# Optimization experiments

Hardware: AMD Instinct MI355X
Metric: run time of the kernel (lower is better)

The kernel has to match this reference:

```python
import jax, jax.numpy as jnp
import numpy as np


def _rope_tables(T, half):
    # theta_i = 10000^(-i/half), standard RoPE frequencies for head_size=2*half
    thetas = 10000.0 ** (-jnp.arange(half, dtype=jnp.float32) / half)  # (half,)
    ang = jnp.arange(T, dtype=jnp.float32)[:, None] * thetas[None, :]  # (T, half)
    return jnp.sin(ang), jnp.cos(ang)


def _apply_rope(x, sin, cos):
    # x: (B, H, T, hs); sin/cos: (T, hs//2). Interleaved pair rotation.
    xe = x[..., 0::2]
    xo = x[..., 1::2]
    s = sin[None, None, :, :]
    c = cos[None, None, :, :]
    re = xe * c - xo * s
    ro = xe * s + xo * c
    return jnp.stack([re, ro], axis=-1).reshape(x.shape)


def setup_inputs() -> dict:
    key = jax.random.key(0)
    ks = jax.random.split(key, 5)
    B, T, C, H = 4, 2048, 1024, 16
    scale = 1.0 / np.sqrt(C)
    x = jax.random.normal(ks[0], (B, T, C), dtype=jnp.float32)
    Wqkv = jax.random.normal(ks[1], (C, 3 * C), dtype=jnp.float32) * scale
    bqkv = jax.random.normal(ks[2], (3 * C,), dtype=jnp.float32) * 0.01
    Wout = jax.random.normal(ks[3], (C, C), dtype=jnp.float32) * scale
    bout = jax.random.normal(ks[4], (C,), dtype=jnp.float32) * 0.01
    return {"x": x, "Wqkv": Wqkv, "bqkv": bqkv, "Wout": Wout, "bout": bout,
            "num_heads": H}


def reference(x, Wqkv, bqkv, Wout, bout, num_heads) -> jnp.ndarray:
    B, T, C = x.shape
    H = num_heads
    hs = C // H
    norm = 1.0 / np.sqrt(hs)

    qkv = x @ Wqkv + bqkv                       # (B, T, 3C)
    qkv = qkv.reshape(B, T, 3, H, hs)
    qkv = jnp.transpose(qkv, (0, 3, 2, 1, 4))   # (B, H, 3, T, hs) = transpose(1,3)
    q, k, v = qkv[:, :, 0], qkv[:, :, 1], qkv[:, :, 2]  # each (B, H, T, hs)

    sin, cos = _rope_tables(T, hs // 2)
    q = _apply_rope(q, sin, cos)
    k = _apply_rope(k, sin, cos)

    att = jnp.einsum('bhqd,bhkd->bhqk', q, k) * norm  # (B, H, T, T)
    causal = jnp.triu(jnp.ones((T, T), dtype=bool), k=1)
    att = jnp.where(causal[None, None], -jnp.inf, att)
    att_prob = jax.nn.softmax(att, axis=-1)

    out = jnp.einsum('bhqk,bhkd->bhqd', att_prob, v)  # (B, H, T, hs)
    out = jnp.transpose(out, (0, 2, 1, 3)).reshape(B, T, C)
    return out @ Wout + bout
```

## Files before the change

kernel.cpp:

```cpp
#include <hip/hip_runtime.h>
#include <math.h>

#define B_   4
#define T_   2048
#define C_   1024
#define H_   16
#define HS   64
#define HALF 32
#define QKV_N (3 * C_)
#define M_    (B_ * T_)

using bf16x8 = __attribute__((ext_vector_type(8))) short;
using f32x4  = __attribute__((ext_vector_type(4))) float;
using f32x16 = __attribute__((ext_vector_type(16))) float;
using u16x4  = __attribute__((ext_vector_type(4))) unsigned short;
using u32x2  = __attribute__((ext_vector_type(2))) unsigned int;

__device__ __forceinline__ unsigned short f2bf(float f) {
    unsigned u = __builtin_bit_cast(unsigned, f);
    u = (u + 0x7FFFu + ((u >> 16) & 1u)) >> 16;
    return (unsigned short)u;
}
__device__ __forceinline__ float bf2f(unsigned short b) {
    return __builtin_bit_cast(float, (unsigned)b << 16);
}
__device__ __forceinline__ unsigned cvtpk_bf16(float lo, float hi_) {
    unsigned r;
    asm("v_cvt_pk_bf16_f32 %0, %1, %2" : "=v"(r) : "v"(lo), "v"(hi_));
    return r;
}
__device__ __forceinline__ void gload16(const void* g, void* l) {
    __builtin_amdgcn_global_load_lds(
        (const __attribute__((address_space(1))) unsigned int*)g,
        (__attribute__((address_space(3))) unsigned int*)l, 16, 0, 0);
}
#define WAIT_VMCNT_8() asm volatile("s_waitcnt vmcnt(8)" ::: "memory")
#define WAIT_VMCNT_0() asm volatile("s_waitcnt vmcnt(0)" ::: "memory")

#if __has_builtin(__builtin_amdgcn_exp2f)
#define EXP2(x) __builtin_amdgcn_exp2f(x)
#else
#define EXP2(x) exp2f(x)
#endif
#define FMAX3(a, b, c) fmaxf(fmaxf((a), (b)), (c))

#define QSCALE 0.18033688011112042f

__global__ __launch_bounds__(256) void prep_kernel(
    const float* __restrict__ in, unsigned short* __restrict__ out,
    float2* __restrict__ tab)
{
    const int bid = blockIdx.x;
    if (bid < 4096) {
        const size_t i = ((size_t)bid * 256 + threadIdx.x) * 8;
        const float4 a = *reinterpret_cast<const float4*>(&in[i]);
        const float4 b = *reinterpret_cast<const float4*>(&in[i + 4]);
        bf16x8 v;
        v[0] = f2bf(a.x); v[1] = f2bf(a.y); v[2] = f2bf(a.z); v[3] = f2bf(a.w);
        v[4] = f2bf(b.x); v[5] = f2bf(b.y); v[6] = f2bf(b.z); v[7] = f2bf(b.w);
        *reinterpret_cast<bf16x8*>(&out[i]) = v;
    } else {
        const int idx = (bid - 4096) * 256 + threadIdx.x;
        const int t = idx / HALF;
        const int i = idx % HALF;
        const float theta = powf(10000.0f, -(float)i / (float)HALF);
        const float ang = (float)t * theta;
        float sn, cs;
        sincosf(ang, &sn, &cs);
        tab[idx] = make_float2(sn, cs);
    }
}

__global__ __launch_bounds__(256) void wtrans_kernel(
    const float* __restrict__ Wqkv, const float* __restrict__ Wout,
    unsigned short* __restrict__ Wqkvt, unsigned short* __restrict__ Woutt)
{
    __shared__ float tile[32][33];
    const int bid = blockIdx.x;
    const float* W;
    unsigned short* Wt;
    int N, k0, n0;
    if (bid < 3072) {
        W = Wqkv; Wt = Wqkvt; N = QKV_N;
        n0 = (bid % 96) * 32; k0 = (bid / 96) * 32;
    } else {
        const int r2 = bid - 3072;
        W = Wout; Wt = Woutt; N = C_;
        n0 = (r2 % 32) * 32; k0 = (r2 / 32) * 32;
    }
    const int K = C_;
    const int r = threadIdx.x / 32;
    const int c = threadIdx.x % 32;
    #pragma unroll
    for (int it = 0; it < 4; ++it)
        tile[r + it * 8][c] = W[(size_t)(k0 + r + it * 8) * N + n0 + c];
    __syncthreads();
    #pragma unroll
    for (int it = 0; it < 4; ++it)
        Wt[(size_t)(n0 + r + it * 8) * K + k0 + c] = f2bf(tile[c][r + it * 8]);
}

template <int N, int K, bool BF16OUT, bool ROPE, bool VSPLIT>
__global__ __launch_bounds__(256, 4) void gemm_mfma_kernel(
    const unsigned short* __restrict__ A, const unsigned short* __restrict__ Bt,
    const float* __restrict__ bias, const float2* __restrict__ tab,
    void* __restrict__ Cout, unsigned short* __restrict__ vt, int nbx, int nby)
{
    __shared__ unsigned short As[128 * 32];
    __shared__ unsigned short Bs[128 * 32];

    const int tid  = threadIdx.x;
    const int lane = tid & 63;
    const int wave = tid >> 6;
    const int wr   = wave >> 1;
    const int wc   = wave & 1;
    const int l15  = lane & 15;
    const int l4   = lane >> 4;

    const int bid  = blockIdx.x;
    const int xcd  = bid & 7;
    const int w    = bid >> 3;
    const int cpr  = nbx >> 1;
    const int rpr  = nby >> 2;
    const int by   = ((xcd >> 1) * rpr) + (w / cpr);
    const int bx   = ((xcd & 1) * cpr) + (w % cpr);
    const int row0 = by * 128;
    const int col0 = bx * 128;

    f32x4 acc[4][4] = {};

    const int ar = tid >> 2, ac = (tid & 3) * 8;
    const unsigned short* ap = &A[(size_t)(row0 + ar) * K + ac];
    const unsigned short* bp = &Bt[(size_t)(col0 + ar) * K + ac];

    for (int it = 0; it < K / 32; ++it) {
        gload16(ap,          &As[tid * 8]);
        gload16(ap + 64 * K, &As[(tid + 256) * 8]);
        gload16(bp,          &Bs[tid * 8]);
        gload16(bp + 64 * K, &Bs[(tid + 256) * 8]);
        __syncthreads();

        bf16x8 a[4], b[4];
        #pragma unroll
        for (int mi = 0; mi < 4; ++mi)
            a[mi] = *reinterpret_cast<const bf16x8*>(
                &As[(wr * 64 + mi * 16 + l15) * 32 + l4 * 8]);
        #pragma unroll
        for (int nj = 0; nj < 4; ++nj)
            b[nj] = *reinterpret_cast<const bf16x8*>(
                &Bs[(wc * 64 + nj * 16 + l15) * 32 + l4 * 8]);
        #pragma unroll
        for (int mi = 0; mi < 4; ++mi)
            #pragma unroll
            for (int nj = 0; nj < 4; ++nj)
                acc[mi][nj] = __builtin_amdgcn_mfma_f32_16x16x32_bf16(
                    a[mi], b[nj], acc[mi][nj], 0, 0, 0);
        __syncthreads();
        ap += 32;
        bp += 32;
    }

    float bv[4];
    #pragma unroll
    for (int nj = 0; nj < 4; ++nj)
        bv[nj] = bias[col0 + wc * 64 + nj * 16 + l15];

    if (VSPLIT && col0 >= 2 * C_) {
        #pragma unroll
        for (int mi = 0; mi < 4; ++mi) {
            const int rowb = row0 + wr * 64 + mi * 16 + l4 * 4;
            const int b  = rowb >> 11;
            const int t0 = rowb & (T_ - 1);
            #pragma unroll
            for (int nj = 0; nj < 4; ++nj) {
                const int cv = col0 - 2 * C_ + wc * 64 + nj * 16 + l15;
                u16x4 pack;
                #pragma unroll
                for (int r = 0; r < 4; ++r)
                    pack[r] = f2bf(acc[mi][nj][r] + bv[nj]);
                *reinterpret_cast<u16x4*>(
                    &vt[((size_t)(b * H_ * HS + cv)) * T_ + t0]) = pack;
            }
        }
        return;
    }

    const bool doRope = ROPE && (col0 < 2 * C_);
    const bool doScaleQ = ROPE && (col0 < C_);

    #pragma unroll
    for (int mi = 0; mi < 4; ++mi) {
        #pragma unroll
        for (int r = 0; r < 4; ++r) {
            const int row = row0 + wr * 64 + mi * 16 + l4 * 4 + r;
            const int t   = row & (T_ - 1);
            #pragma unroll
            for (int nj = 0; nj < 4; ++nj) {
                const int col = col0 + wc * 64 + nj * 16 + l15;
                float v = acc[mi][nj][r] + bv[nj];
                if (doRope) {
                    const float partner = __shfl_xor(v, 1);
                    const float2 sc = tab[t * HALF + ((col & 63) >> 1)];
                    v = v * sc.y + ((col & 1) ? partner : -partner) * sc.x;
                }
                if (doScaleQ) v *= QSCALE;
                if (BF16OUT)
                    ((unsigned short*)Cout)[(size_t)row * N + col] = f2bf(v);
                else
                    ((float*)Cout)[(size_t)row * N + col] = v;
            }
        }
    }
}

__global__ __launch_bounds__(256, 2) void attn_mfma5_kernel(
    const unsigned short* __restrict__ qkv,
    const unsigned short* __restrict__ vt,
    unsigned short* __restrict__ out)
{
    __shared__ unsigned short Ks[2][128 * 64];
    __shared__ unsigned short Vs[2][64 * 128];

    const int idx = blockIdx.x;
    const int bh  = idx & 63;
    const int qp  = idx >> 6;
    const int b   = bh >> 4;
    const int h   = bh & 15;
    const int qtA = qp;
    const int qtB = 15 - qp;

    const int tid  = threadIdx.x;
    const int lane = tid & 63;
    const int w    = tid >> 6;
    const int l31  = lane & 31;
    const int hi   = lane >> 5;

    const int qwA = qtA * 128 + w * 32;
    const int qgA = qwA + l31;
    const int qwB = qtB * 128 + w * 32;
    const int qgB = qwB + l31;

    bf16x8 aqA[4], aqB[4];
    {
        const unsigned short* qpA = &qkv[(size_t)(b * T_ + qgA) * QKV_N + h * HS + hi * 8];
        const unsigned short* qpB = &qkv[(size_t)(b * T_ + qgB) * QKV_N + h * HS + hi * 8];
        #pragma unroll
        for (int kc = 0; kc < 4; ++kc) {
            aqA[kc] = *reinterpret_cast<const bf16x8*>(qpA + kc * 16);
            aqB[kc] = *reinterpret_cast<const bf16x8*>(qpB + kc * 16);
        }
    }

    f32x16 accA0 = {}, accA1 = {}, accB0 = {}, accB1 = {};
    float mA = -INFINITY, lA = 0.f, mB = -INFINITY, lB = 0.f;

    auto stageKV = [&](int buf, int it) {
        #pragma unroll
        for (int n = 0; n < 4; ++n) {
            const int r  = n * 32 + (tid >> 3);
            const int sk = ((tid & 7) ^ (r & 7)) * 8;
            gload16(&qkv[(size_t)(b * T_ + it * 128 + r) * QKV_N + C_ + h * HS + sk],
                    &Ks[buf][(n * 256 + tid) * 8]);
        }
        #pragma unroll
        for (int n = 0; n < 4; ++n) {
            const int d  = n * 16 + (tid >> 4);
            const int sv = ((tid & 15) ^ (d & 7)) * 8;
            gload16(&vt[((size_t)(bh * HS + d)) * T_ + it * 128 + sv],
                    &Vs[buf][(n * 256 + tid) * 8]);
        }
    };

    auto process = [&](const unsigned short* Kb, const unsigned short* Vb,
                       const bf16x8* aq, f32x16& a0, f32x16& a1,
                       float& mval, float& lval, int qw, int qg, int kbase) {
        f32x16 s[4] = {};
        __builtin_amdgcn_s_setprio(1);
        #pragma unroll
        for (int kc = 0; kc < 4; ++kc) {
            const int bo = kc * 32 + hi * 16;
            #pragma unroll
            for (int g = 0; g < 4; ++g) {
                const int rj = g * 32 + l31;
                const bf16x8 ak = *reinterpret_cast<const bf16x8*>(
                    &Kb[rj * 64 + ((bo ^ ((rj & 7) << 4)) >> 1)]);
                s[g] = __builtin_amdgcn_mfma_f32_32x32x16_bf16(ak, aq[kc], s[g], 0, 0, 0);
            }
        }
        __builtin_amdgcn_s_setprio(0);

        if (kbase + 127 > qw) {
            #pragma unroll
            for (int g = 0; g < 4; ++g) {
                #pragma unroll
                for (int r = 0; r < 16; ++r) {
                    const int j0 = kbase + g * 32 + (r & 3) + 8 * (r >> 2) + 4 * hi;
                    if (j0 > qg) s[g][r] = -INFINITY;
                }
            }
        }

        float tg[4];
        #pragma unroll
        for (int g = 0; g < 4; ++g) {
            const float v0 = FMAX3(s[g][0],  s[g][1],  s[g][2]);
            const float v1 = FMAX3(s[g][3],  s[g][4],  s[g][5]);
            const float v2 = FMAX3(s[g][6],  s[g][7],  s[g][8]);
            const float v3 = FMAX3(s[g][9],  s[g][10], s[g][11]);
            const float v4 = FMAX3(s[g][12], s[g][13], s[g][14]);
            tg[g] = fmaxf(FMAX3(v0, v1, v2), FMAX3(v3, v4, s[g][15]));
        }
        float tm = fmaxf(fmaxf(tg[0], tg[1]), fmaxf(tg[2], tg[3]));
        tm = fmaxf(tm, __shfl_xor(tm, 32));

        const bool upd = (tm > mval + 8.f);
        if (__ballot(upd)) {
            const float nm = upd ? tm : mval;
            const float sf = EXP2(mval - nm);
            lval *= sf;
            #pragma unroll
            for (int r = 0; r < 16; ++r) { a0[r] *= sf; a1[r] *= sf; }
            mval = nm;
        }

        float rs0 = 0.f, rs1 = 0.f, rs2 = 0.f, rs3 = 0.f;
        #pragma unroll
        for (int r = 0; r < 16; ++r) {
            s[0][r] = EXP2(s[0][r] - mval); rs0 += s[0][r];
            s[1][r] = EXP2(s[1][r] - mval); rs1 += s[1][r];
            s[2][r] = EXP2(s[2][r] - mval); rs2 += s[2][r];
            s[3][r] = EXP2(s[3][r] - mval); rs3 += s[3][r];
        }
        float rs = (rs0 + rs1) + (rs2 + rs3);
        rs += __shfl_xor(rs, 32);
        lval += rs;

        #pragma unroll
        for (int g2 = 0; g2 < 2; ++g2) {
            #pragma unroll
            for (int jt = 0; jt < 2; ++jt) {
                const int g = g2 * 2 + jt;
                #pragma unroll
                for (int c = 0; c < 2; ++c) {
                    const int e = c * 8;
                    const unsigned pa = cvtpk_bf16(s[g][e + 0], s[g][e + 1]);
                    const unsigned pb = cvtpk_bf16(s[g][e + 2], s[g][e + 3]);
                    const unsigned pc = cvtpk_bf16(s[g][e + 4], s[g][e + 5]);
                    const unsigned pd = cvtpk_bf16(s[g][e + 6], s[g][e + 7]);
                    int4 bw;
#if __has_builtin(__builtin_amdgcn_permlane32_swap)
                    const u32x2 rx = __builtin_amdgcn_permlane32_swap(pa, pc, false, false);
                    const u32x2 ry = __builtin_amdgcn_permlane32_swap(pb, pd, false, false);
                    bw.x = (int)rx[0]; bw.y = (int)ry[0];
                    bw.z = (int)rx[1]; bw.w = (int)ry[1];
#else
                    const unsigned pas = (unsigned)__shfl_xor((int)pa, 32);
                    const unsigned pbs = (unsigned)__shfl_xor((int)pb, 32);
                    const unsigned pcs = (unsigned)__shfl_xor((int)pc, 32);
                    const unsigned pds = (unsigned)__shfl_xor((int)pd, 32);
                    bw.x = (int)(hi ? pcs : pa);
                    bw.y = (int)(hi ? pds : pb);
                    bw.z = (int)(hi ? pc  : pas);
                    bw.w = (int)(hi ? pd  : pbs);
#endif
                    const bf16x8 bfrag = __builtin_bit_cast(bf16x8, bw);

                    const int lslot = g2 * 8 + (jt * 2 + c) * 2 + hi;
                    const int d0 = l31;
                    const bf16x8 av0 = *reinterpret_cast<const bf16x8*>(
                        &Vb[d0 * 128 + (lslot ^ (d0 & 7)) * 8]);
                    const int d1 = 32 + l31;
                    const bf16x8 av1 = *reinterpret_cast<const bf16x8*>(
                        &Vb[d1 * 128 + (lslot ^ (d1 & 7)) * 8]);
                    __builtin_amdgcn_s_setprio(1);
                    a0 = __builtin_amdgcn_mfma_f32_32x32x16_bf16(av0, bfrag, a0, 0, 0, 0);
                    a1 = __builtin_amdgcn_mfma_f32_32x32x16_bf16(av1, bfrag, a1, 0, 0, 0);
                    __builtin_amdgcn_s_setprio(0);
                }
            }
        }
    };

    const int nIter = qtB + 1;
    stageKV(0, 0);
    for (int it = 0; it < nIter; ++it) {
        const int cur = it & 1;
        __builtin_amdgcn_sched_barrier(0);
        if (it + 1 < nIter) {
            stageKV(cur ^ 1, it + 1);
            WAIT_VMCNT_8();
        } else {
            WAIT_VMCNT_0();
        }
        __builtin_amdgcn_s_barrier();
        __builtin_amdgcn_sched_barrier(0);

        const unsigned short* Kb = &Ks[cur][0];
        const unsigned short* Vb = &Vs[cur][0];
        const int kbase = it * 128;
        if (kbase <= qwA + 31)
            process(Kb, Vb, aqA, accA0, accA1, mA, lA, qwA, qgA, kbase);
        if (kbase <= qwB + 31)
            process(Kb, Vb, aqB, accB0, accB1, mB, lB, qwB, qgB, kbase);
        __builtin_amdgcn_sched_barrier(0);
        __builtin_amdgcn_s_barrier();
    }

    {
        const float inv = 1.0f / lA;
        unsigned short* orow = &out[(size_t)(b * T_ + qgA) * C_ + h * HS];
        #pragma unroll
        for (int g = 0; g < 4; ++g) {
            uint2 wv;
            wv.x = cvtpk_bf16(accA0[4 * g + 0] * inv, accA0[4 * g + 1] * inv);
            wv.y = cvtpk_bf16(accA0[4 * g + 2] * inv, accA0[4 * g + 3] * inv);
            *reinterpret_cast<uint2*>(&orow[8 * g + 4 * hi]) = wv;
            uint2 wv1;
            wv1.x = cvtpk_bf16(accA1[4 * g + 0] * inv, accA1[4 * g + 1] * inv);
            wv1.y = cvtpk_bf16(accA1[4 * g + 2] * inv, accA1[4 * g + 3] * inv);
            *reinterpret_cast<uint2*>(&orow[32 + 8 * g + 4 * hi]) = wv1;
        }
    }
    {
        const float inv = 1.0f / lB;
        unsigned short* orow = &out[(size_t)(b * T_ + qgB) * C_ + h * HS];
        #pragma unroll
        for (int g = 0; g < 4; ++g) {
            uint2 wv;
            wv.x = cvtpk_bf16(accB0[4 * g + 0] * inv, accB0[4 * g + 1] * inv);
            wv.y = cvtpk_bf16(accB0[4 * g + 2] * inv, accB0[4 * g + 3] * inv);
            *reinterpret_cast<uint2*>(&orow[8 * g + 4 * hi]) = wv;
            uint2 wv1;
            wv1.x = cvtpk_bf16(accB1[4 * g + 0] * inv, accB1[4 * g + 1] * inv);
            wv1.y = cvtpk_bf16(accB1[4 * g + 2] * inv, accB1[4 * g + 3] * inv);
            *reinterpret_cast<uint2*>(&orow[32 + 8 * g + 4 * hi]) = wv1;
        }
    }
}

extern "C" void kernel_launch(void* const* d_in, const int* in_sizes, int n_in,
                              void* d_out, int out_size, void* d_ws, size_t ws_size,
                              hipStream_t stream)
{
    const float* x    = (const float*)d_in[0];
    const float* Wqkv = (const float*)d_in[1];
    const float* bqkv = (const float*)d_in[2];
    const float* Wout = (const float*)d_in[3];
    const float* bout = (const float*)d_in[4];
    float* out = (float*)d_out;

    char* ws = (char*)d_ws;
    unsigned short* qkvb  = (unsigned short*)ws;
    unsigned short* xb    = (unsigned short*)(ws + 50331648);
    unsigned short* attnb = (unsigned short*)(ws + 67108864);
    unsigned short* vt_g  = (unsigned short*)(ws + 83886080);
    unsigned short* Wqkvt = (unsigned short*)(ws + 100663296);
    unsigned short* Woutt = (unsigned short*)(ws + 106954752);
    float2* tab           = (float2*)(ws + 109051904);

    prep_kernel<<<4352, 256, 0, stream>>>(x, xb, tab);
    wtrans_kernel<<<4096, 256, 0, stream>>>(Wqkv, Wout, Wqkvt, Woutt);

    gemm_mfma_kernel<QKV_N, C_, true, true, true>
        <<<(M_ / 128) * (QKV_N / 128), 256, 0, stream>>>(
        xb, Wqkvt, bqkv, tab, qkvb, vt_g, QKV_N / 128, M_ / 128);

    attn_mfma5_kernel<<<B_ * H_ * (T_ / 256), 256, 0, stream>>>(qkvb, vt_g, attnb);

    gemm_mfma_kernel<C_, C_, false, false, false>
        <<<(M_ / 128) * (C_ / 128), 256, 0, stream>>>(
        attnb, Woutt, bout, nullptr, out, nullptr, C_ / 128, M_ / 128);
}
```

Before: 169.8 us.

## Double-buffer GEMM LDS tiles with swizzle and merge prep kernels

Gives the MFMA GEMM two LDS buffers so the next K-tile's global-to-LDS loads are issued before the current tile's compute, using vmcnt waits and raw barriers instead of __syncthreads. It also XOR-swizzles the LDS column chunk to reduce bank conflicts on fragment reads. Separately, it merges the x conversion, RoPE table and weight transpose kernels into one launch. The cost is double the LDS per block, which may lower occupancy at the declared 4 blocks per CU, and the vmcnt and barrier ordering has to stay exactly right.

```diff
diff --git a/kernel.cpp b/kernel.cpp
--- a/kernel.cpp
+++ b/kernel.cpp
@@ -35,6 +35,7 @@
         (__attribute__((address_space(3))) unsigned int*)l, 16, 0, 0);
 }
 #define WAIT_VMCNT_8() asm volatile("s_waitcnt vmcnt(8)" ::: "memory")
+#define WAIT_VMCNT_4() asm volatile("s_waitcnt vmcnt(4)" ::: "memory")
 #define WAIT_VMCNT_0() asm volatile("s_waitcnt vmcnt(0)" ::: "memory")
 
 #if __has_builtin(__builtin_amdgcn_exp2f)
@@ -46,20 +47,25 @@
 
 #define QSCALE 0.18033688011112042f
 
-__global__ __launch_bounds__(256) void prep_kernel(
-    const float* __restrict__ in, unsigned short* __restrict__ out,
-    float2* __restrict__ tab)
+__global__ __launch_bounds__(256) void prep2_kernel(
+    const float* __restrict__ x, unsigned short* __restrict__ xb,
+    float2* __restrict__ tab,
+    const float* __restrict__ Wqkv, const float* __restrict__ Wout,
+    unsigned short* __restrict__ Wqkvt, unsigned short* __restrict__ Woutt)
 {
+    __shared__ float tile[32][33];
     const int bid = blockIdx.x;
     if (bid < 4096) {
         const size_t i = ((size_t)bid * 256 + threadIdx.x) * 8;
-        const float4 a = *reinterpret_cast<const float4*>(&in[i]);
-        const float4 b = *reinterpret_cast<const float4*>(&in[i + 4]);
+        const float4 a = *reinterpret_cast<const float4*>(&x[i]);
+        const float4 b = *reinterpret_cast<const float4*>(&x[i + 4]);
         bf16x8 v;
         v[0] = f2bf(a.x); v[1] = f2bf(a.y); v[2] = f2bf(a.z); v[3] = f2bf(a.w);
         v[4] = f2bf(b.x); v[5] = f2bf(b.y); v[6] = f2bf(b.z); v[7] = f2bf(b.w);
-        *reinterpret_cast<bf16x8*>(&out[i]) = v;
-    } else {
+        *reinterpret_cast<bf16x8*>(&xb[i]) = v;
+        return;
+    }
+    if (bid < 4352) {
         const int idx = (bid - 4096) * 256 + threadIdx.x;
         const int t = idx / HALF;
         const int i = idx % HALF;
@@ -68,25 +74,19 @@
         float sn, cs;
         sincosf(ang, &sn, &cs);
         tab[idx] = make_float2(sn, cs);
-    }
-}
-
-__global__ __launch_bounds__(256) void wtrans_kernel(
-    const float* __restrict__ Wqkv, const float* __restrict__ Wout,
-    unsigned short* __restrict__ Wqkvt, unsigned short* __restrict__ Woutt)
-{
-    __shared__ float tile[32][33];
-    const int bid = blockIdx.x;
+        return;
+    }
     const float* W;
     unsigned short* Wt;
     int N, k0, n0;
-    if (bid < 3072) {
+    if (bid < 7424) {
+        const int r0 = bid - 4352;
         W = Wqkv; Wt = Wqkvt; N = QKV_N;
-        n0 = (bid % 96) * 32; k0 = (bid / 96) * 32;
+        n0 = (r0 % 96) * 32; k0 = (r0 / 96) * 32;
     } else {
-        const int r2 = bid - 3072;
+        const int r0 = bid - 7424;
         W = Wout; Wt = Woutt; N = C_;
-        n0 = (r2 % 32) * 32; k0 = (r2 / 32) * 32;
+        n0 = (r0 % 32) * 32; k0 = (r0 / 32) * 32;
     }
     const int K = C_;
     const int r = threadIdx.x / 32;
@@ -106,8 +106,8 @@
     const float* __restrict__ bias, const float2* __restrict__ tab,
     void* __restrict__ Cout, unsigned short* __restrict__ vt, int nbx, int nby)
 {
-    __shared__ unsigned short As[128 * 32];
-    __shared__ unsigned short Bs[128 * 32];
+    __shared__ unsigned short As[2][128 * 32];
+    __shared__ unsigned short Bs[2][128 * 32];
 
     const int tid  = threadIdx.x;
     const int lane = tid & 63;
@@ -129,35 +129,63 @@
 
     f32x4 acc[4][4] = {};
 
-    const int ar = tid >> 2, ac = (tid & 3) * 8;
-    const unsigned short* ap = &A[(size_t)(row0 + ar) * K + ac];
-    const unsigned short* bp = &Bt[(size_t)(col0 + ar) * K + ac];
-
-    for (int it = 0; it < K / 32; ++it) {
-        gload16(ap,          &As[tid * 8]);
-        gload16(ap + 64 * K, &As[(tid + 256) * 8]);
-        gload16(bp,          &Bs[tid * 8]);
-        gload16(bp + 64 * K, &Bs[(tid + 256) * 8]);
-        __syncthreads();
+    const int ar  = tid >> 2;
+    const int sl  = tid & 3;
+    const int swz = (sl ^ ((ar >> 1) & 3)) * 8;
+    const unsigned short* ap = &A[(size_t)(row0 + ar) * K + swz];
+    const unsigned short* bp = &Bt[(size_t)(col0 + ar) * K + swz];
+
+    auto stage = [&](int buf, int t) {
+        const unsigned short* a0 = ap + t * 32;
+        const unsigned short* b0 = bp + t * 32;
+        gload16(a0,          &As[buf][tid * 8]);
+        gload16(a0 + 64 * K, &As[buf][(tid + 256) * 8]);
+        gload16(b0,          &Bs[buf][tid * 8]);
+        gload16(b0 + 64 * K, &Bs[buf][(tid + 256) * 8]);
+    };
+
+    int aoff[4], boff[4];
+    #pragma unroll
+    for (int mi = 0; mi < 4; ++mi) {
+        const int lr = wr * 64 + mi * 16 + l15;
+        aoff[mi] = lr * 32 + ((l4 ^ ((lr >> 1) & 3)) * 8);
+    }
+    #pragma unroll
+    for (int nj = 0; nj < 4; ++nj) {
+        const int lr = wc * 64 + nj * 16 + l15;
+        boff[nj] = lr * 32 + ((l4 ^ ((lr >> 1) & 3)) * 8);
+    }
+
+    constexpr int nt = K / 32;
+    stage(0, 0);
+
+    for (int t = 0; t < nt; ++t) {
+        const int cur = t & 1;
+        if (t + 1 < nt) {
+            stage(cur ^ 1, t + 1);
+            WAIT_VMCNT_4();
+        } else {
+            WAIT_VMCNT_0();
+        }
+        __builtin_amdgcn_s_barrier();
+        __builtin_amdgcn_sched_barrier(0);
 
         bf16x8 a[4], b[4];
         #pragma unroll
         for (int mi = 0; mi < 4; ++mi)
-            a[mi] = *reinterpret_cast<const bf16x8*>(
-                &As[(wr * 64 + mi * 16 + l15) * 32 + l4 * 8]);
+            a[mi] = *reinterpret_cast<const bf16x8*>(&As[cur][aoff[mi]]);
         #pragma unroll
         for (int nj = 0; nj < 4; ++nj)
-            b[nj] = *reinterpret_cast<const bf16x8*>(
-                &Bs[(wc * 64 + nj * 16 + l15) * 32 + l4 * 8]);
+            b[nj] = *reinterpret_cast<const bf16x8*>(&Bs[cur][boff[nj]]);
         #pragma unroll
         for (int mi = 0; mi < 4; ++mi)
             #pragma unroll
             for (int nj = 0; nj < 4; ++nj)
                 acc[mi][nj] = __builtin_amdgcn_mfma_f32_16x16x32_bf16(
                     a[mi], b[nj], acc[mi][nj], 0, 0, 0);
-        __syncthreads();
-        ap += 32;
-        bp += 32;
+
+        __builtin_amdgcn_sched_barrier(0);
+        __builtin_amdgcn_s_barrier();
     }
 
     float bv[4];
@@ -458,8 +486,7 @@
     unsigned short* Woutt = (unsigned short*)(ws + 106954752);
     float2* tab           = (float2*)(ws + 109051904);
 
-    prep_kernel<<<4352, 256, 0, stream>>>(x, xb, tab);
-    wtrans_kernel<<<4096, 256, 0, stream>>>(Wqkv, Wout, Wqkvt, Woutt);
+    prep2_kernel<<<8448, 256, 0, stream>>>(x, xb, tab, Wqkv, Wout, Wqkvt, Woutt);
 
     gemm_mfma_kernel<QKV_N, C_, true, true, true>
         <<<(M_ / 128) * (QKV_N / 128), 256, 0, stream>>>(
```

New measurement: 167.2 us. No clear change (-1.5%).
